# Optimization experiments

Measured on AMD Instinct MI355X. Metric: run time of the kernel, lower is better.

Reference implementation:

```python
import jax, jax.numpy as jnp
import numpy as np
import math

B, S, HID, H = 1, 512, 256, 8
D = HID // H
SCALE = 1.0 / math.sqrt(D)
PI = math.pi


def setup_inputs() -> dict:
    key = jax.random.key(0)
    ks = jax.random.split(key, 6)
    x = jax.random.normal(ks[0], (B, S, HID), dtype=jnp.float32)
    w = lambda k: jax.random.normal(k, (HID, HID), dtype=jnp.float32) * 0.02
    return {
        'x': x,
        'wq': w(ks[1]), 'bq': jnp.zeros((HID,), jnp.float32),
        'wk': w(ks[2]), 'bk': jnp.zeros((HID,), jnp.float32),
        'wv': w(ks[3]), 'bv': jnp.zeros((HID,), jnp.float32),
        'wo': w(ks[4]), 'bo': jnp.zeros((HID,), jnp.float32),
    }


def _split_heads(t):
    # [B,S,HID] -> [B,H,S,D]
    return t.reshape(B, S, H, D).transpose(0, 2, 1, 3)


def reference(x, wq, bq, wk, bk, wv, bv, wo, bo):
    # Linear projections (torch nn.Linear: x @ W.T + b)
    q = _split_heads(x @ wq.T + bq)
    k = _split_heads(x @ wk.T + bk)
    v = _split_heads(x @ wv.T + bv)

    omega = jax.nn.sigmoid(q) * PI      # [B,H,S,D]
    amplitude = jax.nn.sigmoid(k)       # [B,H,S,D]
    phase = jnp.tanh(v) * PI            # [B,H,S,D]

    # relative position i-j, [S,S]
    pos = (jnp.arange(S)[:, None] - jnp.arange(S)[None, :]).astype(jnp.float32)
    # wave interference tensor [B,H,S,D,S] (query i, dim d, key j)
    interaction = amplitude[..., None] * jnp.cos(
        omega[..., None] * pos[None, None, :, None, :] + phase[..., None])
    patterns = jax.nn.softmax(interaction * SCALE, axis=-1)  # softmax over keys j
    # contract over key positions: per-dim attention
    context = jnp.einsum('bhidj,bhjd->bhid', patterns, v)    # [B,H,S,D]
    context = context.transpose(0, 2, 1, 3).reshape(B, S, HID)
    return context @ wo.T + bo
```

## Files before the change

kernel.cpp:

```cpp
#include <hip/hip_runtime.h>
#include <math.h>

#define SEQ 512
#define HID 256
#define NH 8
#define DH 32
#define PI_F 3.14159265358979323846f
#define SCALE_F 0.17677669529663687f
#define LOG2E_F 1.4426950408889634f

#define OFF_OMEGA 0
#define OFF_AMP   131072
#define OFF_PHASE 262144
#define OFF_V     393216
#define OFF_CTX   524288

__device__ __forceinline__ void gemm_tile(
    const float* __restrict__ A, const float* __restrict__ W,
    int r0, int c0, int tid, float (&acc)[4][4],
    float* __restrict__ xs, float* __restrict__ wts)
{
#pragma unroll
    for (int i = 0; i < 4; i++)
#pragma unroll
        for (int j = 0; j < 4; j++) acc[i][j] = 0.f;

    const int rg = tid >> 4, cg = tid & 15;

    for (int k0 = 0; k0 < HID; k0 += 64) {
#pragma unroll
        for (int it = 0; it < 4; it++) {
            int idx = tid + it * 256;
            int rr = idx >> 4, f4 = idx & 15;
            float4 av = *(const float4*)(A + (r0 + rr) * HID + k0 + 4 * f4);
            *(float4*)&xs[rr * 68 + 4 * f4] = av;
            float4 wv = *(const float4*)(W + (c0 + rr) * HID + k0 + 4 * f4);
            int cw = rr ^ ((f4 & 7) << 2);
            wts[(4 * f4 + 0) * 64 + cw] = wv.x;
            wts[(4 * f4 + 1) * 64 + cw] = wv.y;
            wts[(4 * f4 + 2) * 64 + cw] = wv.z;
            wts[(4 * f4 + 3) * 64 + cw] = wv.w;
        }
        __syncthreads();
#pragma unroll
        for (int g = 0; g < 16; g++) {
            float xfa[4][4], wfa[4][4];
#pragma unroll
            for (int i = 0; i < 4; i++) {
                float4 xv = *(const float4*)&xs[(4 * rg + i) * 68 + 4 * g];
                xfa[i][0] = xv.x; xfa[i][1] = xv.y; xfa[i][2] = xv.z; xfa[i][3] = xv.w;
            }
            const int sw = (g & 7) << 2;
#pragma unroll
            for (int m = 0; m < 4; m++) {
                float4 wv = *(const float4*)&wts[(4 * g + m) * 64 + ((4 * cg) ^ sw)];
                wfa[m][0] = wv.x; wfa[m][1] = wv.y; wfa[m][2] = wv.z; wfa[m][3] = wv.w;
            }
#pragma unroll
            for (int m = 0; m < 4; m++)
#pragma unroll
                for (int i = 0; i < 4; i++)
#pragma unroll
                    for (int j = 0; j < 4; j++)
                        acc[i][j] = fmaf(xfa[i][m], wfa[m][j], acc[i][j]);
        }
        __syncthreads();
    }
}

__global__ __launch_bounds__(256) void gemm_qkv_act(
    const float* __restrict__ x,
    const float* __restrict__ wq, const float* __restrict__ bq,
    const float* __restrict__ wk, const float* __restrict__ bk,
    const float* __restrict__ wv, const float* __restrict__ bv,
    float* __restrict__ ws)
{
    const int which = blockIdx.y;
    const float* W = (which == 0) ? wq : (which == 1) ? wk : wv;
    const float* B = (which == 0) ? bq : (which == 1) ? bk : bv;
    const int ct = blockIdx.x & 3;
    const int rt = blockIdx.x >> 2;
    const int r0 = rt * 64, c0 = ct * 64;

    __shared__ float xs[64 * 68];
    __shared__ float wts[64 * 64];

    const int tid = threadIdx.x;
    float acc[4][4];
    gemm_tile(x, W, r0, c0, tid, acc, xs, wts);

    const int rg = tid >> 4, cg = tid & 15;
    float4 b4 = *(const float4*)(B + c0 + 4 * cg);
    float bb[4] = {b4.x, b4.y, b4.z, b4.w};

#pragma unroll
    for (int i = 0; i < 4; i++) {
        int row = r0 + 4 * rg + i;
#pragma unroll
        for (int j = 0; j < 4; j++) {
            float val = acc[i][j] + bb[j];
            int o = row * HID + c0 + 4 * cg + j;
            if (which == 0) {
                ws[OFF_OMEGA + o] = PI_F / (1.f + expf(-val));
            } else if (which == 1) {
                ws[OFF_AMP + o] = 1.f / (1.f + expf(-val));
            } else {
                ws[OFF_V + o] = val;
                ws[OFF_PHASE + o] = PI_F * tanhf(val);
            }
        }
    }
}

__global__ __launch_bounds__(256) void gemm_out(
    const float* __restrict__ ctx, const float* __restrict__ wo,
    const float* __restrict__ bo, float* __restrict__ out)
{
    const int ct = blockIdx.x & 3;
    const int rt = blockIdx.x >> 2;
    const int r0 = rt * 64, c0 = ct * 64;

    __shared__ float xs[64 * 68];
    __shared__ float wts[64 * 64];

    const int tid = threadIdx.x;
    float acc[4][4];
    gemm_tile(ctx, wo, r0, c0, tid, acc, xs, wts);

    const int rg = tid >> 4, cg = tid & 15;
    float4 b4 = *(const float4*)(bo + c0 + 4 * cg);
#pragma unroll
    for (int i = 0; i < 4; i++) {
        int row = r0 + 4 * rg + i;
        float4 o;
        o.x = acc[i][0] + b4.x;
        o.y = acc[i][1] + b4.y;
        o.z = acc[i][2] + b4.z;
        o.w = acc[i][3] + b4.w;
        *(float4*)&out[row * HID + c0 + 4 * cg] = o;
    }
}

__global__ __launch_bounds__(256) void wave_attn(const float* __restrict__ ws,
                                                 float* __restrict__ ctx)
{
    const int h  = blockIdx.y;
    const int il = threadIdx.x >> 5;
    const int d  = threadIdx.x & 31;
    const int i  = blockIdx.x * 8 + il;
    const int col = h * DH + d;

    const float w  = ws[OFF_OMEGA + i * HID + col];
    const float aL = ws[OFF_AMP + i * HID + col] * (SCALE_F * LOG2E_F);
    const float ph = ws[OFF_PHASE + i * HID + col];
    const float* vcol = ws + OFF_V + col;

    float sw_, cw;
    sincosf(w, &sw_, &cw);
    float c2 = cw * cw - sw_ * sw_, s2 = 2.f * sw_ * cw;
    float c4 = c2 * c2 - s2 * s2,   s4 = 2.f * s2 * c2;

    float th0 = fmaf(w, (float)i, ph);
    float s0, cc0;
    sincosf(th0, &s0, &cc0);

    float pc[4], psn[4];
    pc[0] = cc0; psn[0] = s0;
#pragma unroll
    for (int k = 1; k < 4; k++) {
        float nc = pc[k - 1] * cw + psn[k - 1] * sw_;
        float ns = psn[k - 1] * cw - pc[k - 1] * sw_;
        pc[k] = nc; psn[k] = ns;
    }
    float p[4], q[4], den[4], num[4];
#pragma unroll
    for (int k = 0; k < 4; k++) {
        p[k] = aL * pc[k]; q[k] = aL * psn[k];
        den[k] = 0.f; num[k] = 0.f;
    }

#pragma unroll 4
    for (int t = 0; t < SEQ / 4; t++) {
        float v0 = vcol[(4 * t + 0) * HID];
        float v1 = vcol[(4 * t + 1) * HID];
        float v2v = vcol[(4 * t + 2) * HID];
        float v3 = vcol[(4 * t + 3) * HID];
        float e0 = __builtin_amdgcn_exp2f(p[0]);
        float e1 = __builtin_amdgcn_exp2f(p[1]);
        float e2 = __builtin_amdgcn_exp2f(p[2]);
        float e3 = __builtin_amdgcn_exp2f(p[3]);
        den[0] += e0; den[1] += e1; den[2] += e2; den[3] += e3;
        num[0] = fmaf(e0, v0, num[0]);
        num[1] = fmaf(e1, v1, num[1]);
        num[2] = fmaf(e2, v2v, num[2]);
        num[3] = fmaf(e3, v3, num[3]);
#pragma unroll
        for (int k = 0; k < 4; k++) {
            float np = p[k] * c4 + q[k] * s4;
            float nq = q[k] * c4 - p[k] * s4;
            p[k] = np; q[k] = nq;
        }
    }
    float denom = (den[0] + den[1]) + (den[2] + den[3]);
    float numer = (num[0] + num[1]) + (num[2] + num[3]);
    ctx[i * HID + col] = numer / denom;
}

extern "C" void kernel_launch(void* const* d_in, const int* in_sizes, int n_in,
                              void* d_out, int out_size, void* d_ws, size_t ws_size,
                              hipStream_t stream) {
    const float* x  = (const float*)d_in[0];
    const float* wq = (const float*)d_in[1];
    const float* bq = (const float*)d_in[2];
    const float* wk = (const float*)d_in[3];
    const float* bk = (const float*)d_in[4];
    const float* wv = (const float*)d_in[5];
    const float* bv = (const float*)d_in[6];
    const float* wo = (const float*)d_in[7];
    const float* bo = (const float*)d_in[8];

    float* ws = (float*)d_ws;

    hipLaunchKernelGGL(gemm_qkv_act, dim3(32, 3), dim3(256), 0, stream,
                       x, wq, bq, wk, bk, wv, bv, ws);
    hipLaunchKernelGGL(wave_attn, dim3(SEQ / 8, NH), dim3(256), 0, stream,
                       ws, ws + OFF_CTX);
    hipLaunchKernelGGL(gemm_out, dim3(32), dim3(256), 0, stream,
                       ws + OFF_CTX, wo, bo, (float*)d_out);
}
```

Baseline: 116.1 us.

## Fuse all stages into one cooperative kernel with split-K GEMMs and grid syncs

Replaces the three separate launches with a single cooperative kernel of 256 blocks. Stages are separated by grid-wide barriers. The QKV and output projections use split-K, writing partial sums to the workspace, and a separate elementwise pass sums them and applies bias and activations. This removes launch gaps and spreads the small GEMMs over more blocks. In exchange it adds four grid syncs, extra workspace traffic for the partial sums, and ties the attention stage to a fixed 256-block grid, each block handling two units.

Result: slower. 236.7 us (+103.8%).

```diff
diff --git a/kernel.cpp b/kernel.cpp
--- a/kernel.cpp
+++ b/kernel.cpp
@@ -1,5 +1,8 @@
 #include <hip/hip_runtime.h>
+#include <hip/hip_cooperative_groups.h>
 #include <math.h>
+
+namespace cg = cooperative_groups;
 
 #define SEQ 512
 #define HID 256
@@ -14,196 +17,215 @@
 #define OFF_PHASE 262144
 #define OFF_V     393216
 #define OFF_CTX   524288
-
-__device__ __forceinline__ void gemm_tile(
+#define OFF_PQ    655360
+#define OFF_PO    1441792
+
+__device__ __forceinline__ void gemm_chunk(
     const float* __restrict__ A, const float* __restrict__ W,
-    int r0, int c0, int tid, float (&acc)[4][4],
+    int r0, int c0, int k0, int tid, float (&acc)[4][4],
     float* __restrict__ xs, float* __restrict__ wts)
 {
 #pragma unroll
-    for (int i = 0; i < 4; i++)
-#pragma unroll
-        for (int j = 0; j < 4; j++) acc[i][j] = 0.f;
-
-    const int rg = tid >> 4, cg = tid & 15;
-
-    for (int k0 = 0; k0 < HID; k0 += 64) {
-#pragma unroll
-        for (int it = 0; it < 4; it++) {
-            int idx = tid + it * 256;
-            int rr = idx >> 4, f4 = idx & 15;
-            float4 av = *(const float4*)(A + (r0 + rr) * HID + k0 + 4 * f4);
-            *(float4*)&xs[rr * 68 + 4 * f4] = av;
-            float4 wv = *(const float4*)(W + (c0 + rr) * HID + k0 + 4 * f4);
-            int cw = rr ^ ((f4 & 7) << 2);
-            wts[(4 * f4 + 0) * 64 + cw] = wv.x;
-            wts[(4 * f4 + 1) * 64 + cw] = wv.y;
-            wts[(4 * f4 + 2) * 64 + cw] = wv.z;
-            wts[(4 * f4 + 3) * 64 + cw] = wv.w;
-        }
-        __syncthreads();
-#pragma unroll
-        for (int g = 0; g < 16; g++) {
-            float xfa[4][4], wfa[4][4];
-#pragma unroll
-            for (int i = 0; i < 4; i++) {
-                float4 xv = *(const float4*)&xs[(4 * rg + i) * 68 + 4 * g];
-                xfa[i][0] = xv.x; xfa[i][1] = xv.y; xfa[i][2] = xv.z; xfa[i][3] = xv.w;
-            }
-            const int sw = (g & 7) << 2;
-#pragma unroll
-            for (int m = 0; m < 4; m++) {
-                float4 wv = *(const float4*)&wts[(4 * g + m) * 64 + ((4 * cg) ^ sw)];
-                wfa[m][0] = wv.x; wfa[m][1] = wv.y; wfa[m][2] = wv.z; wfa[m][3] = wv.w;
-            }
-#pragma unroll
-            for (int m = 0; m < 4; m++)
-#pragma unroll
-                for (int i = 0; i < 4; i++)
-#pragma unroll
-                    for (int j = 0; j < 4; j++)
-                        acc[i][j] = fmaf(xfa[i][m], wfa[m][j], acc[i][j]);
-        }
-        __syncthreads();
-    }
+    for (int it = 0; it < 4; it++) {
+        int idx = tid + it * 256;
+        int rr = idx >> 4, f4 = idx & 15;
+        float4 av = *(const float4*)(A + (r0 + rr) * HID + k0 + 4 * f4);
+        *(float4*)&xs[rr * 68 + 4 * f4] = av;
+        float4 wv = *(const float4*)(W + (c0 + rr) * HID + k0 + 4 * f4);
+        int cw = rr ^ ((f4 & 7) << 2);
+        wts[(4 * f4 + 0) * 64 + cw] = wv.x;
+        wts[(4 * f4 + 1) * 64 + cw] = wv.y;
+        wts[(4 * f4 + 2) * 64 + cw] = wv.z;
+        wts[(4 * f4 + 3) * 64 + cw] = wv.w;
+    }
+    __syncthreads();
+    const int rg = tid >> 4, cgi = tid & 15;
+#pragma unroll
+    for (int g = 0; g < 16; g++) {
+        float xfa[4][4], wfa[4][4];
+#pragma unroll
+        for (int i = 0; i < 4; i++) {
+            float4 xv = *(const float4*)&xs[(4 * rg + i) * 68 + 4 * g];
+            xfa[i][0] = xv.x; xfa[i][1] = xv.y; xfa[i][2] = xv.z; xfa[i][3] = xv.w;
+        }
+        const int sw = (g & 7) << 2;
+#pragma unroll
+        for (int m = 0; m < 4; m++) {
+            float4 wv = *(const float4*)&wts[(4 * g + m) * 64 + ((4 * cgi) ^ sw)];
+            wfa[m][0] = wv.x; wfa[m][1] = wv.y; wfa[m][2] = wv.z; wfa[m][3] = wv.w;
+        }
+#pragma unroll
+        for (int m = 0; m < 4; m++)
+#pragma unroll
+            for (int i = 0; i < 4; i++)
+#pragma unroll
+                for (int j = 0; j < 4; j++)
+                    acc[i][j] = fmaf(xfa[i][m], wfa[m][j], acc[i][j]);
+    }
+    __syncthreads();
 }
 
-__global__ __launch_bounds__(256) void gemm_qkv_act(
+__global__ __launch_bounds__(256, 1) void mega(
     const float* __restrict__ x,
     const float* __restrict__ wq, const float* __restrict__ bq,
     const float* __restrict__ wk, const float* __restrict__ bk,
     const float* __restrict__ wv, const float* __restrict__ bv,
-    float* __restrict__ ws)
+    const float* __restrict__ wo, const float* __restrict__ bo,
+    float* __restrict__ ws, float* __restrict__ out)
 {
-    const int which = blockIdx.y;
-    const float* W = (which == 0) ? wq : (which == 1) ? wk : wv;
-    const float* B = (which == 0) ? bq : (which == 1) ? bk : bv;
-    const int ct = blockIdx.x & 3;
-    const int rt = blockIdx.x >> 2;
-    const int r0 = rt * 64, c0 = ct * 64;
+    cg::grid_group grid = cg::this_grid();
+    const int tid = threadIdx.x;
+    const int b = blockIdx.x;
 
     __shared__ float xs[64 * 68];
     __shared__ float wts[64 * 64];
 
-    const int tid = threadIdx.x;
-    float acc[4][4];
-    gemm_tile(x, W, r0, c0, tid, acc, xs, wts);
-
-    const int rg = tid >> 4, cg = tid & 15;
-    float4 b4 = *(const float4*)(B + c0 + 4 * cg);
-    float bb[4] = {b4.x, b4.y, b4.z, b4.w};
-
-#pragma unroll
-    for (int i = 0; i < 4; i++) {
-        int row = r0 + 4 * rg + i;
-#pragma unroll
-        for (int j = 0; j < 4; j++) {
-            float val = acc[i][j] + bb[j];
-            int o = row * HID + c0 + 4 * cg + j;
+    if (b < 192) {
+        const int ks = b & 1;
+        const int tile = b >> 1;
+        const int which = tile >> 5;
+        const int t = tile & 31;
+        const int r0 = (t >> 2) * 64, c0 = (t & 3) * 64, k0 = ks * 128;
+        const float* W = (which == 0) ? wq : (which == 1) ? wk : wv;
+        float acc[4][4];
+#pragma unroll
+        for (int i = 0; i < 4; i++)
+#pragma unroll
+            for (int j = 0; j < 4; j++) acc[i][j] = 0.f;
+        gemm_chunk(x, W, r0, c0, k0,      tid, acc, xs, wts);
+        gemm_chunk(x, W, r0, c0, k0 + 64, tid, acc, xs, wts);
+        float* P = ws + OFF_PQ + (which * 2 + ks) * (SEQ * HID);
+        const int rg = tid >> 4, cgi = tid & 15;
+#pragma unroll
+        for (int i = 0; i < 4; i++) {
+            float4 o4 = {acc[i][0], acc[i][1], acc[i][2], acc[i][3]};
+            *(float4*)&P[(r0 + 4 * rg + i) * HID + c0 + 4 * cgi] = o4;
+        }
+    }
+    grid.sync();
+
+    {
+        const int gtid = b * 256 + tid;
+#pragma unroll
+        for (int s = 0; s < 6; s++) {
+            int idx = gtid + s * 65536;
+            int which = idx >> 17;
+            int o = idx & 131071;
+            int c = idx & 255;
+            const float* P = ws + OFF_PQ + which * 2 * (SEQ * HID) + o;
+            float v = P[0] + P[SEQ * HID];
             if (which == 0) {
-                ws[OFF_OMEGA + o] = PI_F / (1.f + expf(-val));
+                v += bq[c];
+                ws[OFF_OMEGA + o] = PI_F / (1.f + expf(-v));
             } else if (which == 1) {
-                ws[OFF_AMP + o] = 1.f / (1.f + expf(-val));
+                v += bk[c];
+                ws[OFF_AMP + o] = 1.f / (1.f + expf(-v));
             } else {
-                ws[OFF_V + o] = val;
-                ws[OFF_PHASE + o] = PI_F * tanhf(val);
-            }
-        }
-    }
-}
-
-__global__ __launch_bounds__(256) void gemm_out(
-    const float* __restrict__ ctx, const float* __restrict__ wo,
-    const float* __restrict__ bo, float* __restrict__ out)
-{
-    const int ct = blockIdx.x & 3;
-    const int rt = blockIdx.x >> 2;
-    const int r0 = rt * 64, c0 = ct * 64;
-
-    __shared__ float xs[64 * 68];
-    __shared__ float wts[64 * 64];
-
-    const int tid = threadIdx.x;
-    float acc[4][4];
-    gemm_tile(ctx, wo, r0, c0, tid, acc, xs, wts);
-
-    const int rg = tid >> 4, cg = tid & 15;
-    float4 b4 = *(const float4*)(bo + c0 + 4 * cg);
-#pragma unroll
-    for (int i = 0; i < 4; i++) {
-        int row = r0 + 4 * rg + i;
-        float4 o;
-        o.x = acc[i][0] + b4.x;
-        o.y = acc[i][1] + b4.y;
-        o.z = acc[i][2] + b4.z;
-        o.w = acc[i][3] + b4.w;
-        *(float4*)&out[row * HID + c0 + 4 * cg] = o;
-    }
-}
-
-__global__ __launch_bounds__(256) void wave_attn(const float* __restrict__ ws,
-                                                 float* __restrict__ ctx)
-{
-    const int h  = blockIdx.y;
-    const int il = threadIdx.x >> 5;
-    const int d  = threadIdx.x & 31;
-    const int i  = blockIdx.x * 8 + il;
-    const int col = h * DH + d;
-
-    const float w  = ws[OFF_OMEGA + i * HID + col];
-    const float aL = ws[OFF_AMP + i * HID + col] * (SCALE_F * LOG2E_F);
-    const float ph = ws[OFF_PHASE + i * HID + col];
-    const float* vcol = ws + OFF_V + col;
-
-    float sw_, cw;
-    sincosf(w, &sw_, &cw);
-    float c2 = cw * cw - sw_ * sw_, s2 = 2.f * sw_ * cw;
-    float c4 = c2 * c2 - s2 * s2,   s4 = 2.f * s2 * c2;
-
-    float th0 = fmaf(w, (float)i, ph);
-    float s0, cc0;
-    sincosf(th0, &s0, &cc0);
-
-    float pc[4], psn[4];
-    pc[0] = cc0; psn[0] = s0;
-#pragma unroll
-    for (int k = 1; k < 4; k++) {
-        float nc = pc[k - 1] * cw + psn[k - 1] * sw_;
-        float ns = psn[k - 1] * cw - pc[k - 1] * sw_;
-        pc[k] = nc; psn[k] = ns;
-    }
-    float p[4], q[4], den[4], num[4];
-#pragma unroll
-    for (int k = 0; k < 4; k++) {
-        p[k] = aL * pc[k]; q[k] = aL * psn[k];
-        den[k] = 0.f; num[k] = 0.f;
-    }
-
+                v += bv[c];
+                ws[OFF_V + o] = v;
+                ws[OFF_PHASE + o] = PI_F * tanhf(v);
+            }
+        }
+    }
+    grid.sync();
+
+    {
+        const int il = tid >> 5;
+        const int d = tid & 31;
+#pragma unroll
+        for (int r = 0; r < 2; r++) {
+            const int u = b * 2 + r;
+            const int i8 = u >> 3;
+            const int h = u & 7;
+            const int i = i8 * 8 + il;
+            const int col = h * DH + d;
+
+            const float w  = ws[OFF_OMEGA + i * HID + col];
+            const float aL = ws[OFF_AMP + i * HID + col] * (SCALE_F * LOG2E_F);
+            const float ph = ws[OFF_PHASE + i * HID + col];
+            const float* vcol = ws + OFF_V + col;
+
+            float sw_, cw;
+            sincosf(w, &sw_, &cw);
+            float c2 = cw * cw - sw_ * sw_, s2 = 2.f * sw_ * cw;
+            float c4 = c2 * c2 - s2 * s2,   s4 = 2.f * s2 * c2;
+
+            float th0 = fmaf(w, (float)i, ph);
+            float s0, cc0;
+            sincosf(th0, &s0, &cc0);
+
+            float pc[4], psn[4];
+            pc[0] = cc0; psn[0] = s0;
+#pragma unroll
+            for (int k = 1; k < 4; k++) {
+                float nc = pc[k - 1] * cw + psn[k - 1] * sw_;
+                float ns = psn[k - 1] * cw - pc[k - 1] * sw_;
+                pc[k] = nc; psn[k] = ns;
+            }
+            float p[4], q[4], den[4], num[4];
+#pragma unroll
+            for (int k = 0; k < 4; k++) {
+                p[k] = aL * pc[k]; q[k] = aL * psn[k];
+                den[k] = 0.f; num[k] = 0.f;
+            }
 #pragma unroll 4
-    for (int t = 0; t < SEQ / 4; t++) {
-        float v0 = vcol[(4 * t + 0) * HID];
-        float v1 = vcol[(4 * t + 1) * HID];
-        float v2v = vcol[(4 * t + 2) * HID];
-        float v3 = vcol[(4 * t + 3) * HID];
-        float e0 = __builtin_amdgcn_exp2f(p[0]);
-        float e1 = __builtin_amdgcn_exp2f(p[1]);
-        float e2 = __builtin_amdgcn_exp2f(p[2]);
-        float e3 = __builtin_amdgcn_exp2f(p[3]);
-        den[0] += e0; den[1] += e1; den[2] += e2; den[3] += e3;
-        num[0] = fmaf(e0, v0, num[0]);
-        num[1] = fmaf(e1, v1, num[1]);
-        num[2] = fmaf(e2, v2v, num[2]);
-        num[3] = fmaf(e3, v3, num[3]);
-#pragma unroll
-        for (int k = 0; k < 4; k++) {
-            float np = p[k] * c4 + q[k] * s4;
-            float nq = q[k] * c4 - p[k] * s4;
-            p[k] = np; q[k] = nq;
-        }
-    }
-    float denom = (den[0] + den[1]) + (den[2] + den[3]);
-    float numer = (num[0] + num[1]) + (num[2] + num[3]);
-    ctx[i * HID + col] = numer / denom;
+            for (int t4 = 0; t4 < SEQ / 4; t4++) {
+                float v0 = vcol[(4 * t4 + 0) * HID];
+                float v1 = vcol[(4 * t4 + 1) * HID];
+                float v2 = vcol[(4 * t4 + 2) * HID];
+                float v3 = vcol[(4 * t4 + 3) * HID];
+                float e0 = __builtin_amdgcn_exp2f(p[0]);
+                float e1 = __builtin_amdgcn_exp2f(p[1]);
+                float e2 = __builtin_amdgcn_exp2f(p[2]);
+                float e3 = __builtin_amdgcn_exp2f(p[3]);
+                den[0] += e0; den[1] += e1; den[2] += e2; den[3] += e3;
+                num[0] = fmaf(e0, v0, num[0]);
+                num[1] = fmaf(e1, v1, num[1]);
+                num[2] = fmaf(e2, v2, num[2]);
+                num[3] = fmaf(e3, v3, num[3]);
+#pragma unroll
+                for (int k = 0; k < 4; k++) {
+                    float np = p[k] * c4 + q[k] * s4;
+                    float nq = q[k] * c4 - p[k] * s4;
+                    p[k] = np; q[k] = nq;
+                }
+            }
+            float denom = (den[0] + den[1]) + (den[2] + den[3]);
+            float numer = (num[0] + num[1]) + (num[2] + num[3]);
+            ws[OFF_CTX + i * HID + col] = numer / denom;
+        }
+    }
+    grid.sync();
+
+    if (b < 128) {
+        const int tile = b >> 2, ks = b & 3;
+        const int r0 = (tile >> 2) * 64, c0 = (tile & 3) * 64, k0 = ks * 64;
+        float acc[4][4];
+#pragma unroll
+        for (int i = 0; i < 4; i++)
+#pragma unroll
+            for (int j = 0; j < 4; j++) acc[i][j] = 0.f;
+        gemm_chunk(ws + OFF_CTX, wo, r0, c0, k0, tid, acc, xs, wts);
+        float* P = ws + OFF_PO + ks * (SEQ * HID);
+        const int rg = tid >> 4, cgi = tid & 15;
+#pragma unroll
+        for (int i = 0; i < 4; i++) {
+            float4 o4 = {acc[i][0], acc[i][1], acc[i][2], acc[i][3]};
+            *(float4*)&P[(r0 + 4 * rg + i) * HID + c0 + 4 * cgi] = o4;
+        }
+    }
+    grid.sync();
+
+    {
+        const int gtid = b * 256 + tid;
+#pragma unroll
+        for (int s = 0; s < 2; s++) {
+            int idx = gtid + s * 65536;
+            const float* P = ws + OFF_PO + idx;
+            out[idx] = (P[0] + P[SEQ * HID]) + (P[2 * SEQ * HID] + P[3 * SEQ * HID])
+                       + bo[idx & 255];
+        }
+    }
 }
 
 extern "C" void kernel_launch(void* const* d_in, const int* in_sizes, int n_in,
@@ -218,13 +240,12 @@
     const float* bv = (const float*)d_in[6];
     const float* wo = (const float*)d_in[7];
     const float* bo = (const float*)d_in[8];
-
-    float* ws = (float*)d_ws;
-
-    hipLaunchKernelGGL(gemm_qkv_act, dim3(32, 3), dim3(256), 0, stream,
-                       x, wq, bq, wk, bk, wv, bv, ws);
-    hipLaunchKernelGGL(wave_attn, dim3(SEQ / 8, NH), dim3(256), 0, stream,
-                       ws, ws + OFF_CTX);
-    hipLaunchKernelGGL(gemm_out, dim3(32), dim3(256), 0, stream,
-                       ws + OFF_CTX, wo, bo, (float*)d_out);
+    float* ws  = (float*)d_ws;
+    float* out = (float*)d_out;
+
+    void* args[] = {(void*)&x, (void*)&wq, (void*)&bq, (void*)&wk, (void*)&bk,
+                    (void*)&wv, (void*)&bv, (void*)&wo, (void*)&bo,
+                    (void*)&ws, (void*)&out};
+    hipLaunchCooperativeKernel((const void*)mega, dim3(256), dim3(256),
+                               args, 0, stream);
 }
```

## Shrink GEMM tiles to launch more blocks and use row-major weight tiles

Applied to the files above, without the earlier changes.

Both GEMM kernels now use smaller output tiles (64x32 for QKV, 32x32 for output projection), so the QKV launch goes from 96 to 192 blocks and the output launch from 32 to 128. This fills more of the GPU's compute units for these small matrices. Weights are now stored in shared memory row-major with padding and read as dot-product float4s, replacing the transposed, swizzled layout. The smaller per-thread tiles lower register reuse and issue more shared-memory reads per FMA, and the final stores become scalar.

After: 112.4 us. -3.3%, faster.

```diff
diff --git a/kernel.cpp b/kernel.cpp
--- a/kernel.cpp
+++ b/kernel.cpp
@@ -15,59 +15,6 @@
 #define OFF_V     393216
 #define OFF_CTX   524288
 
-__device__ __forceinline__ void gemm_tile(
-    const float* __restrict__ A, const float* __restrict__ W,
-    int r0, int c0, int tid, float (&acc)[4][4],
-    float* __restrict__ xs, float* __restrict__ wts)
-{
-#pragma unroll
-    for (int i = 0; i < 4; i++)
-#pragma unroll
-        for (int j = 0; j < 4; j++) acc[i][j] = 0.f;
-
-    const int rg = tid >> 4, cg = tid & 15;
-
-    for (int k0 = 0; k0 < HID; k0 += 64) {
-#pragma unroll
-        for (int it = 0; it < 4; it++) {
-            int idx = tid + it * 256;
-            int rr = idx >> 4, f4 = idx & 15;
-            float4 av = *(const float4*)(A + (r0 + rr) * HID + k0 + 4 * f4);
-            *(float4*)&xs[rr * 68 + 4 * f4] = av;
-            float4 wv = *(const float4*)(W + (c0 + rr) * HID + k0 + 4 * f4);
-            int cw = rr ^ ((f4 & 7) << 2);
-            wts[(4 * f4 + 0) * 64 + cw] = wv.x;
-            wts[(4 * f4 + 1) * 64 + cw] = wv.y;
-            wts[(4 * f4 + 2) * 64 + cw] = wv.z;
-            wts[(4 * f4 + 3) * 64 + cw] = wv.w;
-        }
-        __syncthreads();
-#pragma unroll
-        for (int g = 0; g < 16; g++) {
-            float xfa[4][4], wfa[4][4];
-#pragma unroll
-            for (int i = 0; i < 4; i++) {
-                float4 xv = *(const float4*)&xs[(4 * rg + i) * 68 + 4 * g];
-                xfa[i][0] = xv.x; xfa[i][1] = xv.y; xfa[i][2] = xv.z; xfa[i][3] = xv.w;
-            }
-            const int sw = (g & 7) << 2;
-#pragma unroll
-            for (int m = 0; m < 4; m++) {
-                float4 wv = *(const float4*)&wts[(4 * g + m) * 64 + ((4 * cg) ^ sw)];
-                wfa[m][0] = wv.x; wfa[m][1] = wv.y; wfa[m][2] = wv.z; wfa[m][3] = wv.w;
-            }
-#pragma unroll
-            for (int m = 0; m < 4; m++)
-#pragma unroll
-                for (int i = 0; i < 4; i++)
-#pragma unroll
-                    for (int j = 0; j < 4; j++)
-                        acc[i][j] = fmaf(xfa[i][m], wfa[m][j], acc[i][j]);
-        }
-        __syncthreads();
-    }
-}
-
 __global__ __launch_bounds__(256) void gemm_qkv_act(
     const float* __restrict__ x,
     const float* __restrict__ wq, const float* __restrict__ bq,
@@ -75,31 +22,69 @@
     const float* __restrict__ wv, const float* __restrict__ bv,
     float* __restrict__ ws)
 {
-    const int which = blockIdx.y;
+    const int b = blockIdx.x;
+    const int which = b >> 6;
+    const int t = b & 63;
+    const int r0 = (t >> 3) * 64;
+    const int c0 = (t & 7) * 32;
     const float* W = (which == 0) ? wq : (which == 1) ? wk : wv;
     const float* B = (which == 0) ? bq : (which == 1) ? bk : bv;
-    const int ct = blockIdx.x & 3;
-    const int rt = blockIdx.x >> 2;
-    const int r0 = rt * 64, c0 = ct * 64;
-
-    __shared__ float xs[64 * 68];
-    __shared__ float wts[64 * 64];
+
+    __shared__ float xs[64][68];
+    __shared__ float wls[32][68];
 
     const int tid = threadIdx.x;
-    float acc[4][4];
-    gemm_tile(x, W, r0, c0, tid, acc, xs, wts);
-
     const int rg = tid >> 4, cg = tid & 15;
-    float4 b4 = *(const float4*)(B + c0 + 4 * cg);
-    float bb[4] = {b4.x, b4.y, b4.z, b4.w};
-
+
+    float acc[4][2];
+#pragma unroll
+    for (int i = 0; i < 4; i++) { acc[i][0] = 0.f; acc[i][1] = 0.f; }
+
+    for (int k0 = 0; k0 < HID; k0 += 64) {
+#pragma unroll
+        for (int it = 0; it < 4; it++) {
+            int idx = tid + it * 256;
+            int rr = idx >> 4, f = idx & 15;
+            *(float4*)&xs[rr][4 * f] =
+                *(const float4*)(x + (r0 + rr) * HID + k0 + 4 * f);
+        }
+#pragma unroll
+        for (int it = 0; it < 2; it++) {
+            int idx = tid + it * 256;
+            int cc = idx >> 4, f = idx & 15;
+            *(float4*)&wls[cc][4 * f] =
+                *(const float4*)(W + (c0 + cc) * HID + k0 + 4 * f);
+        }
+        __syncthreads();
+#pragma unroll
+        for (int g = 0; g < 16; g++) {
+            float4 wv0 = *(const float4*)&wls[2 * cg + 0][4 * g];
+            float4 wv1 = *(const float4*)&wls[2 * cg + 1][4 * g];
+#pragma unroll
+            for (int i = 0; i < 4; i++) {
+                float4 xv = *(const float4*)&xs[4 * rg + i][4 * g];
+                acc[i][0] = fmaf(xv.x, wv0.x, acc[i][0]);
+                acc[i][0] = fmaf(xv.y, wv0.y, acc[i][0]);
+                acc[i][0] = fmaf(xv.z, wv0.z, acc[i][0]);
+                acc[i][0] = fmaf(xv.w, wv0.w, acc[i][0]);
+                acc[i][1] = fmaf(xv.x, wv1.x, acc[i][1]);
+                acc[i][1] = fmaf(xv.y, wv1.y, acc[i][1]);
+                acc[i][1] = fmaf(xv.z, wv1.z, acc[i][1]);
+                acc[i][1] = fmaf(xv.w, wv1.w, acc[i][1]);
+            }
+        }
+        __syncthreads();
+    }
+
+    const float b0 = B[c0 + 2 * cg + 0];
+    const float b1 = B[c0 + 2 * cg + 1];
 #pragma unroll
     for (int i = 0; i < 4; i++) {
         int row = r0 + 4 * rg + i;
 #pragma unroll
-        for (int j = 0; j < 4; j++) {
-            float val = acc[i][j] + bb[j];
-            int o = row * HID + c0 + 4 * cg + j;
+        for (int j = 0; j < 2; j++) {
+            float val = acc[i][j] + (j ? b1 : b0);
+            int o = row * HID + c0 + 2 * cg + j;
             if (which == 0) {
                 ws[OFF_OMEGA + o] = PI_F / (1.f + expf(-val));
             } else if (which == 1) {
@@ -112,32 +97,61 @@
     }
 }
 
-__global__ __launch_bounds__(256) void gemm_out(
+__global__ __launch_bounds__(256) void gemm_out_bias(
     const float* __restrict__ ctx, const float* __restrict__ wo,
     const float* __restrict__ bo, float* __restrict__ out)
 {
-    const int ct = blockIdx.x & 3;
-    const int rt = blockIdx.x >> 2;
-    const int r0 = rt * 64, c0 = ct * 64;
-
-    __shared__ float xs[64 * 68];
-    __shared__ float wts[64 * 64];
+    const int b = blockIdx.x;
+    const int r0 = (b >> 3) * 32;
+    const int c0 = (b & 7) * 32;
+
+    __shared__ float xs[32][68];
+    __shared__ float wls[32][68];
 
     const int tid = threadIdx.x;
-    float acc[4][4];
-    gemm_tile(ctx, wo, r0, c0, tid, acc, xs, wts);
-
     const int rg = tid >> 4, cg = tid & 15;
-    float4 b4 = *(const float4*)(bo + c0 + 4 * cg);
-#pragma unroll
-    for (int i = 0; i < 4; i++) {
-        int row = r0 + 4 * rg + i;
-        float4 o;
-        o.x = acc[i][0] + b4.x;
-        o.y = acc[i][1] + b4.y;
-        o.z = acc[i][2] + b4.z;
-        o.w = acc[i][3] + b4.w;
-        *(float4*)&out[row * HID + c0 + 4 * cg] = o;
+
+    float acc[2][2];
+    acc[0][0] = acc[0][1] = acc[1][0] = acc[1][1] = 0.f;
+
+    for (int k0 = 0; k0 < HID; k0 += 64) {
+#pragma unroll
+        for (int it = 0; it < 2; it++) {
+            int idx = tid + it * 256;
+            int rr = idx >> 4, f = idx & 15;
+            *(float4*)&xs[rr][4 * f] =
+                *(const float4*)(ctx + (r0 + rr) * HID + k0 + 4 * f);
+            *(float4*)&wls[rr][4 * f] =
+                *(const float4*)(wo + (c0 + rr) * HID + k0 + 4 * f);
+        }
+        __syncthreads();
+#pragma unroll
+        for (int g = 0; g < 16; g++) {
+            float4 wv0 = *(const float4*)&wls[2 * cg + 0][4 * g];
+            float4 wv1 = *(const float4*)&wls[2 * cg + 1][4 * g];
+#pragma unroll
+            for (int i = 0; i < 2; i++) {
+                float4 xv = *(const float4*)&xs[2 * rg + i][4 * g];
+                acc[i][0] = fmaf(xv.x, wv0.x, acc[i][0]);
+                acc[i][0] = fmaf(xv.y, wv0.y, acc[i][0]);
+                acc[i][0] = fmaf(xv.z, wv0.z, acc[i][0]);
+                acc[i][0] = fmaf(xv.w, wv0.w, acc[i][0]);
+                acc[i][1] = fmaf(xv.x, wv1.x, acc[i][1]);
+                acc[i][1] = fmaf(xv.y, wv1.y, acc[i][1]);
+                acc[i][1] = fmaf(xv.z, wv1.z, acc[i][1]);
+                acc[i][1] = fmaf(xv.w, wv1.w, acc[i][1]);
+            }
+        }
+        __syncthreads();
+    }
+
+    const float b0 = bo[c0 + 2 * cg + 0];
+    const float b1 = bo[c0 + 2 * cg + 1];
+#pragma unroll
+    for (int i = 0; i < 2; i++) {
+        int row = r0 + 2 * rg + i;
+        out[row * HID + c0 + 2 * cg + 0] = acc[i][0] + b0;
+        out[row * HID + c0 + 2 * cg + 1] = acc[i][1] + b1;
     }
 }
 
@@ -221,10 +235,10 @@
 
     float* ws = (float*)d_ws;
 
-    hipLaunchKernelGGL(gemm_qkv_act, dim3(32, 3), dim3(256), 0, stream,
+    hipLaunchKernelGGL(gemm_qkv_act, dim3(192), dim3(256), 0, stream,
                        x, wq, bq, wk, bk, wv, bv, ws);
     hipLaunchKernelGGL(wave_attn, dim3(SEQ / 8, NH), dim3(256), 0, stream,
                        ws, ws + OFF_CTX);
-    hipLaunchKernelGGL(gemm_out, dim3(32), dim3(256), 0, stream,
+    hipLaunchKernelGGL(gemm_out_bias, dim3(128), dim3(256), 0, stream,
                        ws + OFF_CTX, wo, bo, (float*)d_out);
 }
```
